# Kernel tuning notes

Hardware: AMD Instinct MI355X
Metric: run time of the kernel (lower is better)

## Reference

```python
import jax, jax.numpy as jnp
import numpy as np

N, E, B, L = 32768, 524288, 64, 512  # nodes, edges, graphs, max nodes/graph
V, D, H = 10000, 256, 512            # vocab, embed_dim, hidden_dim


def gcn_conv(h, W, b, src, dst, n):
    """PyG GCNConv: add self-loops, symmetric deg normalization, scatter-sum."""
    h = h @ W  # [n, out]
    loops = jnp.arange(n)
    s = jnp.concatenate([src, loops])
    d = jnp.concatenate([dst, loops])
    deg = jax.ops.segment_sum(jnp.ones_like(d, dtype=h.dtype), d, num_segments=n)
    dinv = jnp.where(deg > 0, jax.lax.rsqrt(deg), 0.0)
    norm = dinv[s] * dinv[d]  # [E+n]
    out = jax.ops.segment_sum(h[s] * norm[:, None], d, num_segments=n)
    return out + b


def gru_seq(x, Wih, Whh, bih, bhh):
    """torch nn.GRU (1 layer, batch_first). x: [B, T, H] -> outputs [T, B, H]."""
    def step(h, x_t):
        gi = x_t @ Wih.T + bih          # [B, 3H]
        gh = h @ Whh.T + bhh            # [B, 3H]
        ir, iz, inn = jnp.split(gi, 3, axis=-1)
        hr, hz, hn = jnp.split(gh, 3, axis=-1)
        r = jax.nn.sigmoid(ir + hr)
        z = jax.nn.sigmoid(iz + hz)
        n = jnp.tanh(inn + r * hn)
        h = (1.0 - z) * n + z * h
        return h, h
    h0 = jnp.zeros((x.shape[0], Whh.shape[1]), x.dtype)
    _, outs = jax.lax.scan(step, h0, jnp.swapaxes(x, 0, 1))
    return outs  # [T, B, H]


def setup_inputs() -> dict:
    key = jax.random.key(0)
    ks = jax.random.split(key, 16)
    s = 0.05
    x = jax.random.randint(ks[0], (N,), 0, V)
    edge_index = jax.random.randint(ks[1], (2, E), 0, N)
    batch_idx = jnp.arange(N) // L  # sorted graph ids, L nodes per graph
    focal_points = jax.random.uniform(ks[2], (B, 1), jnp.float32)
    return {
        "x": x, "edge_index": edge_index, "batch_idx": batch_idx,
        "focal_points": focal_points,
        "emb": jax.random.normal(ks[3], (V, D), jnp.float32) * s,
        "W1": jax.random.normal(ks[4], (D, H), jnp.float32) * s,
        "b1": jnp.zeros((H,), jnp.float32),
        "W2": jax.random.normal(ks[5], (H, H), jnp.float32) * s,
        "b2": jnp.zeros((H,), jnp.float32),
        "Wih": jax.random.normal(ks[6], (3 * H, H), jnp.float32) * s,
        "Whh": jax.random.normal(ks[7], (3 * H, H), jnp.float32) * s,
        "bih": jnp.zeros((3 * H,), jnp.float32),
        "bhh": jnp.zeros((3 * H,), jnp.float32),
        "fc1_w": jax.random.normal(ks[8], (H + 1, H), jnp.float32) * s,
        "fc1_b": jnp.zeros((H,), jnp.float32),
        "fc2_w": jax.random.normal(ks[9], (H, 1), jnp.float32) * s,
        "fc2_b": jnp.zeros((1,), jnp.float32),
    }


def reference(x, edge_index, batch_idx, focal_points, emb, W1, b1, W2, b2,
              Wih, Whh, bih, bhh, fc1_w, fc1_b, fc2_w, fc2_b):
    src, dst = edge_index[0], edge_index[1]
    h = emb[x]  # [N, D]
    h = jax.nn.relu(gcn_conv(h, W1, b1, src, dst, N))
    h = jax.nn.relu(gcn_conv(h, W2, b2, src, dst, N))  # [N, H]

    # Ragged -> padded: scatter each node to (graph, position-within-graph)
    ones = jnp.ones((N,), h.dtype)
    counts = jax.ops.segment_sum(ones, batch_idx, num_segments=B)
    starts = jnp.cumsum(counts) - counts  # exclusive cumsum
    pos = jnp.arange(N) - starts[batch_idx].astype(jnp.int32)
    padded = jnp.zeros((B, L, H), h.dtype).at[batch_idx, pos].set(h)

    gru_out = gru_seq(padded, Wih, Whh, bih, bhh)   # [L, B, H]
    graph_emb = gru_out.mean(axis=0)                # [B, H]
    g = jnp.concatenate([graph_emb, focal_points], axis=1)  # [B, H+1]
    out = jax.nn.relu(g @ fc1_w + fc1_b)
    out = jax.nn.sigmoid(out @ fc2_w + fc2_b)       # [B, 1]
    return out
```

## Files before the change

### kernel.cpp

```cpp
#include <hip/hip_runtime.h>

#define NODES 32768
#define EDGES 524288
#define BGR   64
#define LSEQ  512
#define DEMB  256
#define HDIM  512

typedef unsigned short u16;
typedef unsigned int   u32;
typedef unsigned long long u64;
typedef __attribute__((ext_vector_type(8))) short short8;
typedef __attribute__((ext_vector_type(4))) float f32x4;

__device__ __forceinline__ float bf2f(u16 u){ u32 x = ((u32)u)<<16; float f; __builtin_memcpy(&f,&x,4); return f; }
__device__ __forceinline__ u16 f2bf(float f){ u32 x; __builtin_memcpy(&x,&f,4); u32 r = x + 0x7fffu + ((x>>16)&1u); return (u16)(r>>16); }
__device__ __forceinline__ float lo16(u32 u){ u32 x = u<<16; float f; __builtin_memcpy(&f,&x,4); return f; }
__device__ __forceinline__ float hi16(u32 u){ u32 x = u & 0xffff0000u; float f; __builtin_memcpy(&f,&x,4); return f; }
__device__ __forceinline__ u32 pack2(float a, float b){ return (u32)f2bf(a) | ((u32)f2bf(b)<<16); }


__global__ void zero_i32(int* p, int n){
  int i = blockIdx.x*256 + threadIdx.x;
  if (i < n) p[i] = 0;
}

__global__ void transpose_cast(const float* __restrict__ in, u16* __restrict__ out, int K, int N){
  int i = blockIdx.x*256 + threadIdx.x;
  if (i < N*K){ int n = i / K, k = i - n*K; out[i] = f2bf(in[(size_t)k*N + n]); }
}

__global__ void cast_bf(const float* __restrict__ in, u16* __restrict__ out, int n){
  int i = blockIdx.x*256 + threadIdx.x;
  if (i < n) out[i] = f2bf(in[i]);
}

__global__ void count_indeg(const int* __restrict__ dst, int* __restrict__ indeg){
  int e = blockIdx.x*256 + threadIdx.x;
  if (e < EDGES) atomicAdd(&indeg[dst[e]], 1);
}

__global__ void compute_dinv(const int* __restrict__ indeg, float* __restrict__ dinv){
  int i = blockIdx.x*256 + threadIdx.x;
  if (i < NODES) dinv[i] = rsqrtf((float)(indeg[i] + 1));
}

__global__ __launch_bounds__(1024) void scan_csr(const int* __restrict__ indeg,
                                                 int* __restrict__ row_ptr,
                                                 int* __restrict__ cursor){
  __shared__ int part[1024];
  int tid = threadIdx.x, base = tid*32;
  int loc[32]; int s = 0;
  for (int i=0;i<32;i++){ loc[i] = s; s += indeg[base+i]; }
  part[tid] = s; __syncthreads();
  for (int off=1; off<1024; off<<=1){
    int v = part[tid]; int add = (tid>=off) ? part[tid-off] : 0;
    __syncthreads(); part[tid] = v + add; __syncthreads();
  }
  int offt = (tid==0) ? 0 : part[tid-1];
  for (int i=0;i<32;i++){ int v = offt + loc[i]; row_ptr[base+i] = v; cursor[base+i] = v; }
}

__global__ void fill_csr(const int* __restrict__ src, const int* __restrict__ dst,
                         int* __restrict__ cursor, int* __restrict__ csr_src){
  int e = blockIdx.x*256 + threadIdx.x;
  if (e < EDGES){ int d = dst[e]; int p = atomicAdd(&cursor[d], 1); csr_src[p] = src[e]; }
}

__global__ __launch_bounds__(256) void agg_emb(const int* __restrict__ x, const u16* __restrict__ embb,
    const float* __restrict__ dinv, const int* __restrict__ row_ptr, const int* __restrict__ indeg,
    const int* __restrict__ csr_src, u16* __restrict__ out){
  int node = blockIdx.x*4 + (threadIdx.x>>6);
  int lane = threadIdx.x & 63;
  float di = dinv[node];
  int xi = x[node];
  u64 hv = *(const u64*)(embb + (size_t)xi*DEMB + lane*4);
  u32 h0 = (u32)hv, h1 = (u32)(hv>>32);
  float a0 = lo16(h0)*di, a1 = hi16(h0)*di, a2 = lo16(h1)*di, a3 = hi16(h1)*di;
  int st = row_ptr[node], cn = indeg[node];
  for (int p = st; p < st+cn; p++){
    int s = csr_src[p];
    float ws = dinv[s];
    u64 v = *(const u64*)(embb + (size_t)x[s]*DEMB + lane*4);
    u32 w0 = (u32)v, w1 = (u32)(v>>32);
    a0 += lo16(w0)*ws; a1 += hi16(w0)*ws; a2 += lo16(w1)*ws; a3 += hi16(w1)*ws;
  }
  u64 pv = (u64)pack2(a0*di,a1*di) | ((u64)pack2(a2*di,a3*di)<<32);
  *(u64*)(out + (size_t)node*DEMB + lane*4) = pv;
}

__global__ __launch_bounds__(256) void agg_h(const u16* __restrict__ hin, const float* __restrict__ dinv,
    const int* __restrict__ row_ptr, const int* __restrict__ indeg,
    const int* __restrict__ csr_src, u16* __restrict__ out){
  int node = blockIdx.x*4 + (threadIdx.x>>6);
  int lane = threadIdx.x & 63;
  float di = dinv[node];
  float a[8];
  uint4 hv = *((const uint4*)(hin + (size_t)node*HDIM) + lane);
  a[0]=lo16(hv.x)*di; a[1]=hi16(hv.x)*di; a[2]=lo16(hv.y)*di; a[3]=hi16(hv.y)*di;
  a[4]=lo16(hv.z)*di; a[5]=hi16(hv.z)*di; a[6]=lo16(hv.w)*di; a[7]=hi16(hv.w)*di;
  int st = row_ptr[node], cn = indeg[node];
  for (int p = st; p < st+cn; p++){
    int s = csr_src[p];
    float ws = dinv[s];
    uint4 v = *((const uint4*)(hin + (size_t)s*HDIM) + lane);
    a[0]+=lo16(v.x)*ws; a[1]+=hi16(v.x)*ws; a[2]+=lo16(v.y)*ws; a[3]+=hi16(v.y)*ws;
    a[4]+=lo16(v.z)*ws; a[5]+=hi16(v.z)*ws; a[6]+=lo16(v.w)*ws; a[7]+=hi16(v.w)*ws;
  }
  uint4 o; o.x=pack2(a[0]*di,a[1]*di); o.y=pack2(a[2]*di,a[3]*di);
  o.z=pack2(a[4]*di,a[5]*di); o.w=pack2(a[6]*di,a[7]*di);
  *(uint4*)(out + (size_t)node*HDIM + lane*8) = o;
}

#define BM 128
#define BN 128
#define BKK 32
__global__ __launch_bounds__(256) void gemm_bt(const u16* __restrict__ A, const u16* __restrict__ BT,
    const float* __restrict__ bias, u16* __restrict__ C, int M, int N, int K, int relu){
  __shared__ u16 aS[BM][BKK+8];
  __shared__ u16 bS[BN][BKK+8];
  int tid = threadIdx.x;
  int m0 = blockIdx.y * BM, n0 = blockIdx.x * BN;
  int lane = tid & 63, w = tid >> 6;
  int wm = w >> 1, wn = w & 1;
  f32x4 acc[4][4];
  for (int i=0;i<4;i++) for (int j=0;j<4;j++) acc[i][j] = (f32x4)0.0f;

  int r  = tid >> 1;
  int cc = (tid & 1) * 16;
  const u16* Ag = A + (size_t)(m0 + r) * K + cc;
  const u16* Bg = BT + (size_t)(n0 + r) * K + cc;
  int l15 = lane & 15, q8 = (lane >> 4) * 8;

  for (int k0 = 0; k0 < K; k0 += BKK) {
    uint4 av0 = *(const uint4*)(Ag + k0);
    uint4 av1 = *(const uint4*)(Ag + k0 + 8);
    uint4 bv0 = *(const uint4*)(Bg + k0);
    uint4 bv1 = *(const uint4*)(Bg + k0 + 8);
    *(uint4*)&aS[r][cc]   = av0; *(uint4*)&aS[r][cc+8] = av1;
    *(uint4*)&bS[r][cc]   = bv0; *(uint4*)&bS[r][cc+8] = bv1;
    __syncthreads();
    short8 af[4], bfr[4];
    for (int i=0;i<4;i++) af[i]  = *(const short8*)&aS[wm*64 + i*16 + l15][q8];
    for (int j=0;j<4;j++) bfr[j] = *(const short8*)&bS[wn*64 + j*16 + l15][q8];
    for (int i=0;i<4;i++)
      for (int j=0;j<4;j++)
        acc[i][j] = __builtin_amdgcn_mfma_f32_16x16x32_bf16(af[i], bfr[j], acc[i][j], 0, 0, 0);
    __syncthreads();
  }
  int q = lane >> 4;
  for (int i=0;i<4;i++) for (int j=0;j<4;j++){
    int col = n0 + wn*64 + j*16 + l15;
    float bval = bias[col];
    for (int rr=0; rr<4; rr++){
      int row = m0 + wm*64 + i*16 + q*4 + rr;
      float v = acc[i][j][rr] + bval;
      if (relu) v = fmaxf(v, 0.f);
      C[(size_t)row * N + col] = f2bf(v);
    }
  }
}

__global__ __launch_bounds__(512) void gru_kernel(const u16* __restrict__ gi,
    const float* __restrict__ Whh, const float* __restrict__ bhh,
    float* __restrict__ graph_emb, u64* __restrict__ xbuf){
  __shared__ u16  w_lds[96*520];
  __shared__ u16  h_lds[16*520];
  __shared__ float gh_lds[16*100];

  int tid = threadIdx.x;
  int g = blockIdx.x >> 4, j = blockIdx.x & 15;
  int lane = tid & 63, wave = tid >> 6;

  for (int idx = tid; idx < 96*512; idx += 512){
    int rr = idx >> 9, c = idx & 511;
    int grow = (rr >> 5) * 512 + j*32 + (rr & 31);
    w_lds[rr*520 + c] = f2bf(Whh[(size_t)grow*512 + c]);
  }
  for (int idx = tid; idx < 16*520; idx += 512) h_lds[idx] = 0;

  int b = tid >> 5, hh = tid & 31;
  int bg = g*16 + b;
  int c_r = j*32 + hh, c_z = 512 + j*32 + hh, c_n = 1024 + j*32 + hh;
  float bias_r = bhh[c_r], bias_z = bhh[c_z], bias_n = bhh[c_n];
  const u16* gi_row = gi + (size_t)bg * LSEQ * 1536;
  float h_prev = 0.f, accm = 0.f;
  int l15 = lane & 15, q8 = (lane>>4)*8, qr = (lane>>4)*4;

  u64* xb = xbuf + (size_t)g * 8192;
  u16 g_r = gi_row[c_r], g_z = gi_row[c_z], g_n = gi_row[c_n];

  __syncthreads();

  for (int t = 0; t < LSEQ; t++){
    if (wave < 6){
      f32x4 acc0 = (f32x4)0.0f, acc1 = (f32x4)0.0f;
      const u16* wrow = &w_lds[(wave*16 + l15)*520];
      const u16* hrow = &h_lds[l15*520];
      #pragma unroll
      for (int k0 = 0; k0 < 256; k0 += 32){
        acc0 = __builtin_amdgcn_mfma_f32_16x16x32_bf16(*(const short8*)(hrow + k0 + q8),
                                                       *(const short8*)(wrow + k0 + q8), acc0, 0, 0, 0);
        acc1 = __builtin_amdgcn_mfma_f32_16x16x32_bf16(*(const short8*)(hrow + 256 + k0 + q8),
                                                       *(const short8*)(wrow + 256 + k0 + q8), acc1, 0, 0, 0);
      }
      f32x4 acc = acc0 + acc1;
      int col = wave*16 + l15;
      #pragma unroll
      for (int rr2 = 0; rr2 < 4; rr2++) gh_lds[(qr + rr2)*100 + col] = acc[rr2];
    }
    __syncthreads();

    float ghr = gh_lds[b*100 + hh]      + bias_r;
    float ghz = gh_lds[b*100 + 32 + hh] + bias_z;
    float ghn = gh_lds[b*100 + 64 + hh] + bias_n;
    float rg = 1.f / (1.f + __expf(-(bf2f(g_r) + ghr)));
    float zg = 1.f / (1.f + __expf(-(bf2f(g_z) + ghz)));
    float pre = bf2f(g_n) + rg * ghn;
    pre = fminf(fmaxf(pre, -20.f), 20.f);
    float e2 = __expf(2.f * pre);
    float nn = (e2 - 1.f) / (e2 + 1.f);
    float h_new = (1.f - zg) * nn + zg * h_prev;
    accm += h_new; h_prev = h_new;

    u32 tag = (u32)(t + 1);
    float h_nb = __shfl_xor(h_new, 1, 64);
    if ((hh & 1) == 0){
      u64 val = ((u64)tag << 32) | (u64)pack2(h_new, h_nb);
      __hip_atomic_store(xb + (size_t)((t&1)*16 + b)*256 + j*16 + (hh>>1), val,
                         __ATOMIC_RELAXED, __HIP_MEMORY_SCOPE_AGENT);
    }

    int tn = (t + 1 < LSEQ) ? t + 1 : t;
    const u16* gp2 = gi_row + (size_t)tn * 1536;
    u16 n_r = gp2[c_r], n_z = gp2[c_z], n_n = gp2[c_n];

    const u64* rp = xb + (size_t)((t&1)*16 + b)*256 + hh*8;
    u64 v[8];
    bool ok;
    do {
      #pragma unroll
      for (int i=0;i<8;i++) v[i] = __hip_atomic_load(rp + i, __ATOMIC_RELAXED, __HIP_MEMORY_SCOPE_AGENT);
      ok = true;
      #pragma unroll
      for (int i=0;i<8;i++) ok = ok && ((u32)(v[i] >> 32) == tag);
    } while (!ok);

    u32* hl = (u32*)h_lds + b*260 + hh*8;
    #pragma unroll
    for (int i=0;i<8;i++) hl[i] = (u32)v[i];
    __syncthreads();

    g_r = n_r; g_z = n_z; g_n = n_n;
  }
  graph_emb[(size_t)bg*512 + j*32 + hh] = accm * (1.f/512.f);
}

__global__ __launch_bounds__(256) void head(const float* __restrict__ graph_emb, const float* __restrict__ focal,
    const float* __restrict__ fc1w, const float* __restrict__ fc1b,
    const float* __restrict__ fc2w, const float* __restrict__ fc2b, float* __restrict__ out){
  __shared__ float gv[513];
  __shared__ float h1s[512];
  __shared__ float red[4];
  int bq = blockIdx.x, tid = threadIdx.x;
  for (int i = tid; i < 512; i += 256) gv[i] = graph_emb[(size_t)bq*512 + i];
  if (tid == 0) gv[512] = focal[bq];
  __syncthreads();
  for (int c = tid; c < 512; c += 256){
    float acc = fc1b[c];
    for (int k = 0; k < 513; k++) acc += gv[k] * fc1w[(size_t)k*512 + c];
    h1s[c] = fmaxf(acc, 0.f);
  }
  __syncthreads();
  float p = h1s[tid]*fc2w[tid] + h1s[tid+256]*fc2w[tid+256];
  for (int off = 32; off; off >>= 1) p += __shfl_down(p, off, 64);
  if ((tid & 63) == 0) red[tid >> 6] = p;
  __syncthreads();
  if (tid == 0){
    float s = red[0]+red[1]+red[2]+red[3] + fc2b[0];
    out[bq] = 1.f / (1.f + __expf(-s));
  }
}

extern "C" void kernel_launch(void* const* d_in, const int* in_sizes, int n_in,
                              void* d_out, int out_size, void* d_ws, size_t ws_size,
                              hipStream_t stream){
  const int*   x     = (const int*)d_in[0];
  const int*   edge  = (const int*)d_in[1];
  const int*   srcp  = edge;
  const int*   dstp  = edge + EDGES;
  const float* focal = (const float*)d_in[3];
  const float* emb   = (const float*)d_in[4];
  const float* W1    = (const float*)d_in[5];
  const float* b1    = (const float*)d_in[6];
  const float* W2    = (const float*)d_in[7];
  const float* b2    = (const float*)d_in[8];
  const float* Wih   = (const float*)d_in[9];
  const float* Whh   = (const float*)d_in[10];
  const float* bih   = (const float*)d_in[11];
  const float* bhh   = (const float*)d_in[12];
  const float* fc1w  = (const float*)d_in[13];
  const float* fc1b  = (const float*)d_in[14];
  const float* fc2w  = (const float*)d_in[15];
  const float* fc2b  = (const float*)d_in[16];

  char* ws = (char*)d_ws;
  constexpr size_t H2_OFF    = 0;
  constexpr size_t AGG1_OFF  = 33554432;
  constexpr size_t H1_OFF    = 50331648;
  constexpr size_t AGG2_OFF  = 83886080;
  constexpr size_t GI_OFF    = 33554432;
  constexpr size_t MISC      = 134217728;
  constexpr size_t INDEG_OFF = MISC;
  constexpr size_t CNT_OFF   = MISC + 131072;
  constexpr size_t DINV_OFF  = MISC + 131328;
  constexpr size_t ROWPTR_OFF= MISC + 262400;
  constexpr size_t CURSOR_OFF= MISC + 393472;
  constexpr size_t CSR_OFF   = MISC + 524544;
  constexpr size_t W1T_OFF   = MISC + 2621696;
  constexpr size_t W2T_OFF   = MISC + 2883840;
  constexpr size_t WIHB_OFF  = MISC + 3408128;
  constexpr size_t XBUF_OFF  = MISC + 4980992;
  constexpr size_t GEMB_OFF  = MISC + 5243136;

  int*   indeg  = (int*)(ws + INDEG_OFF);
  float* dinv   = (float*)(ws + DINV_OFF);
  int*   rowptr = (int*)(ws + ROWPTR_OFF);
  int*   cursor = (int*)(ws + CURSOR_OFF);
  int*   csrsrc = (int*)(ws + CSR_OFF);
  u16*   W1T    = (u16*)(ws + W1T_OFF);
  u16*   W2T    = (u16*)(ws + W2T_OFF);
  u16*   WihB   = (u16*)(ws + WIHB_OFF);
  u16*   agg1   = (u16*)(ws + AGG1_OFF);
  u16*   h1     = (u16*)(ws + H1_OFF);
  u16*   agg2   = (u16*)(ws + AGG2_OFF);
  u16*   embb   = (u16*)(ws + AGG2_OFF);
  u16*   h2     = (u16*)(ws + H2_OFF);
  u16*   gi     = (u16*)(ws + GI_OFF);
  u64*   xbuf   = (u64*)(ws + XBUF_OFF);
  float* gemb   = (float*)(ws + GEMB_OFF);

  zero_i32<<<129, 256, 0, stream>>>(indeg, 32768 + 64);
  transpose_cast<<<512, 256, 0, stream>>>(W1, W1T, 256, 512);
  transpose_cast<<<1024, 256, 0, stream>>>(W2, W2T, 512, 512);
  cast_bf<<<3072, 256, 0, stream>>>(Wih, WihB, 1536*512);
  cast_bf<<<10000, 256, 0, stream>>>(emb, embb, 10000*256);
  count_indeg<<<2048, 256, 0, stream>>>(dstp, indeg);
  compute_dinv<<<128, 256, 0, stream>>>(indeg, dinv);
  scan_csr<<<1, 1024, 0, stream>>>(indeg, rowptr, cursor);
  fill_csr<<<2048, 256, 0, stream>>>(srcp, dstp, cursor, csrsrc);
  agg_emb<<<8192, 256, 0, stream>>>(x, embb, dinv, rowptr, indeg, csrsrc, agg1);
  gemm_bt<<<dim3(4, 256), 256, 0, stream>>>(agg1, W1T, b1, h1, NODES, 512, 256, 1);
  agg_h<<<8192, 256, 0, stream>>>(h1, dinv, rowptr, indeg, csrsrc, agg2);
  gemm_bt<<<dim3(4, 256), 256, 0, stream>>>(agg2, W2T, b2, h2, NODES, 512, 512, 1);
  gemm_bt<<<dim3(12, 256), 256, 0, stream>>>(h2, WihB, bih, gi, NODES, 1536, 512, 0);
  gru_kernel<<<64, 512, 0, stream>>>(gi, Whh, bhh, gemb, xbuf);
  head<<<64, 256, 0, stream>>>(gemb, focal, fc1w, fc1b, fc2w, fc2b, (float*)d_out);
}
```

Baseline: 2.587 ms.

## Interleave two batch groups per GRU block to hide inter-block exchange latency

```diff
diff --git a/kernel.cpp b/kernel.cpp
--- a/kernel.cpp
+++ b/kernel.cpp
@@ -165,95 +165,131 @@
     const float* __restrict__ Whh, const float* __restrict__ bhh,
     float* __restrict__ graph_emb, u64* __restrict__ xbuf){
   __shared__ u16  w_lds[96*520];
-  __shared__ u16  h_lds[16*520];
-  __shared__ float gh_lds[16*100];
+  __shared__ u16  hA_lds[16*520];
+  __shared__ u16  hB_lds[16*520];
+  __shared__ float ghA_lds[16*100];
+  __shared__ float ghB_lds[16*100];
 
   int tid = threadIdx.x;
-  int g = blockIdx.x >> 4, j = blockIdx.x & 15;
+  int tau = blockIdx.x >> 4, j = blockIdx.x & 15;
+  int gA = tau*2, gB = tau*2 + 1;
   int lane = tid & 63, wave = tid >> 6;
+  (void)lane;
 
   for (int idx = tid; idx < 96*512; idx += 512){
     int rr = idx >> 9, c = idx & 511;
     int grow = (rr >> 5) * 512 + j*32 + (rr & 31);
     w_lds[rr*520 + c] = f2bf(Whh[(size_t)grow*512 + c]);
   }
-  for (int idx = tid; idx < 16*520; idx += 512) h_lds[idx] = 0;
+  for (int idx = tid; idx < 16*520; idx += 512){ hA_lds[idx] = 0; hB_lds[idx] = 0; }
 
   int b = tid >> 5, hh = tid & 31;
-  int bg = g*16 + b;
+  int bgA = gA*16 + b, bgB = gB*16 + b;
   int c_r = j*32 + hh, c_z = 512 + j*32 + hh, c_n = 1024 + j*32 + hh;
   float bias_r = bhh[c_r], bias_z = bhh[c_z], bias_n = bhh[c_n];
-  const u16* gi_row = gi + (size_t)bg * LSEQ * 1536;
-  float h_prev = 0.f, accm = 0.f;
-  int l15 = lane & 15, q8 = (lane>>4)*8, qr = (lane>>4)*4;
-
-  u64* xb = xbuf + (size_t)g * 8192;
-  u16 g_r = gi_row[c_r], g_z = gi_row[c_z], g_n = gi_row[c_n];
+  const u16* giA = gi + (size_t)bgA * LSEQ * 1536;
+  const u16* giB = gi + (size_t)bgB * LSEQ * 1536;
+  float h_prevA = 0.f, accmA = 0.f;
+  float h_prevB = 0.f, accmB = 0.f;
+  int l15 = tid & 15, q8 = ((tid & 63)>>4)*8, qr = ((tid & 63)>>4)*4;
+
+  u64* xbA = xbuf + (size_t)gA * 8192;
+  u64* xbB = xbuf + (size_t)gB * 8192;
+  u16 gA_r = giA[c_r], gA_z = giA[c_z], gA_n = giA[c_n];
+  u16 gB_r = giB[c_r], gB_z = giB[c_z], gB_n = giB[c_n];
 
   __syncthreads();
 
+#define MATVEC(HLDS, GHLDS) do { \
+    f32x4 acc0 = (f32x4)0.0f, acc1 = (f32x4)0.0f; \
+    const u16* wrow = &w_lds[(wave*16 + l15)*520]; \
+    const u16* hrow = &HLDS[l15*520]; \
+    _Pragma("unroll") \
+    for (int k0 = 0; k0 < 256; k0 += 32){ \
+      acc0 = __builtin_amdgcn_mfma_f32_16x16x32_bf16(*(const short8*)(hrow + k0 + q8), \
+                                                     *(const short8*)(wrow + k0 + q8), acc0, 0, 0, 0); \
+      acc1 = __builtin_amdgcn_mfma_f32_16x16x32_bf16(*(const short8*)(hrow + 256 + k0 + q8), \
+                                                     *(const short8*)(wrow + 256 + k0 + q8), acc1, 0, 0, 0); \
+    } \
+    f32x4 acc = acc0 + acc1; \
+    int col = wave*16 + l15; \
+    _Pragma("unroll") \
+    for (int rr2 = 0; rr2 < 4; rr2++) GHLDS[(qr + rr2)*100 + col] = acc[rr2]; \
+  } while(0)
+
+#define GATES(GHLDS, GR, GZ, GN, HPREV, HNEW) do { \
+    float ghr = GHLDS[b*100 + hh]      + bias_r; \
+    float ghz = GHLDS[b*100 + 32 + hh] + bias_z; \
+    float ghn = GHLDS[b*100 + 64 + hh] + bias_n; \
+    float rg = 1.f / (1.f + __expf(-(bf2f(GR) + ghr))); \
+    float zg = 1.f / (1.f + __expf(-(bf2f(GZ) + ghz))); \
+    float pre = bf2f(GN) + rg * ghn; \
+    pre = fminf(fmaxf(pre, -20.f), 20.f); \
+    float e2 = __expf(2.f * pre); \
+    float nn = (e2 - 1.f) / (e2 + 1.f); \
+    HNEW = (1.f - zg) * nn + zg * HPREV; \
+  } while(0)
+
+#define PUBLISH(XB, HNEW) do { \
+    float h_nb = __shfl_xor(HNEW, 1, 64); \
+    if ((hh & 1) == 0){ \
+      u64 val = ((u64)tag << 32) | (u64)pack2(HNEW, h_nb); \
+      __hip_atomic_store(XB + (size_t)((t&1)*16 + b)*256 + j*16 + (hh>>1), val, \
+                         __ATOMIC_RELAXED, __HIP_MEMORY_SCOPE_AGENT); \
+    } \
+  } while(0)
+
+#define POLLCOMMIT(XB, HLDS) do { \
+    const u64* rp = XB + (size_t)((t&1)*16 + b)*256 + hh*8; \
+    u64 v[8]; bool ok; \
+    do { \
+      _Pragma("unroll") \
+      for (int i=0;i<8;i++) v[i] = __hip_atomic_load(rp + i, __ATOMIC_RELAXED, __HIP_MEMORY_SCOPE_AGENT); \
+      ok = true; \
+      _Pragma("unroll") \
+      for (int i=0;i<8;i++) ok = ok && ((u32)(v[i] >> 32) == tag); \
+    } while (!ok); \
+    u32* hl = (u32*)HLDS + b*260 + hh*8; \
+    _Pragma("unroll") \
+    for (int i=0;i<8;i++) hl[i] = (u32)v[i]; \
+  } while(0)
+
   for (int t = 0; t < LSEQ; t++){
-    if (wave < 6){
-      f32x4 acc0 = (f32x4)0.0f, acc1 = (f32x4)0.0f;
-      const u16* wrow = &w_lds[(wave*16 + l15)*520];
-      const u16* hrow = &h_lds[l15*520];
-      #pragma unroll
-      for (int k0 = 0; k0 < 256; k0 += 32){
-        acc0 = __builtin_amdgcn_mfma_f32_16x16x32_bf16(*(const short8*)(hrow + k0 + q8),
-                                                       *(const short8*)(wrow + k0 + q8), acc0, 0, 0, 0);
-        acc1 = __builtin_amdgcn_mfma_f32_16x16x32_bf16(*(const short8*)(hrow + 256 + k0 + q8),
-                                                       *(const short8*)(wrow + 256 + k0 + q8), acc1, 0, 0, 0);
-      }
-      f32x4 acc = acc0 + acc1;
-      int col = wave*16 + l15;
-      #pragma unroll
-      for (int rr2 = 0; rr2 < 4; rr2++) gh_lds[(qr + rr2)*100 + col] = acc[rr2];
-    }
-    __syncthreads();
-
-    float ghr = gh_lds[b*100 + hh]      + bias_r;
-    float ghz = gh_lds[b*100 + 32 + hh] + bias_z;
-    float ghn = gh_lds[b*100 + 64 + hh] + bias_n;
-    float rg = 1.f / (1.f + __expf(-(bf2f(g_r) + ghr)));
-    float zg = 1.f / (1.f + __expf(-(bf2f(g_z) + ghz)));
-    float pre = bf2f(g_n) + rg * ghn;
-    pre = fminf(fmaxf(pre, -20.f), 20.f);
-    float e2 = __expf(2.f * pre);
-    float nn = (e2 - 1.f) / (e2 + 1.f);
-    float h_new = (1.f - zg) * nn + zg * h_prev;
-    accm += h_new; h_prev = h_new;
-
     u32 tag = (u32)(t + 1);
-    float h_nb = __shfl_xor(h_new, 1, 64);
-    if ((hh & 1) == 0){
-      u64 val = ((u64)tag << 32) | (u64)pack2(h_new, h_nb);
-      __hip_atomic_store(xb + (size_t)((t&1)*16 + b)*256 + j*16 + (hh>>1), val,
-                         __ATOMIC_RELAXED, __HIP_MEMORY_SCOPE_AGENT);
-    }
-
     int tn = (t + 1 < LSEQ) ? t + 1 : t;
-    const u16* gp2 = gi_row + (size_t)tn * 1536;
-    u16 n_r = gp2[c_r], n_z = gp2[c_z], n_n = gp2[c_n];
-
-    const u64* rp = xb + (size_t)((t&1)*16 + b)*256 + hh*8;
-    u64 v[8];
-    bool ok;
-    do {
-      #pragma unroll
-      for (int i=0;i<8;i++) v[i] = __hip_atomic_load(rp + i, __ATOMIC_RELAXED, __HIP_MEMORY_SCOPE_AGENT);
-      ok = true;
-      #pragma unroll
-      for (int i=0;i<8;i++) ok = ok && ((u32)(v[i] >> 32) == tag);
-    } while (!ok);
-
-    u32* hl = (u32*)h_lds + b*260 + hh*8;
-    #pragma unroll
-    for (int i=0;i<8;i++) hl[i] = (u32)v[i];
-    __syncthreads();
-
-    g_r = n_r; g_z = n_z; g_n = n_n;
-  }
-  graph_emb[(size_t)bg*512 + j*32 + hh] = accm * (1.f/512.f);
+
+    if (wave < 6) MATVEC(hA_lds, ghA_lds);
+    __syncthreads();
+    float h_newA;
+    GATES(ghA_lds, gA_r, gA_z, gA_n, h_prevA, h_newA);
+    accmA += h_newA; h_prevA = h_newA;
+    PUBLISH(xbA, h_newA);
+    const u16* gpA = giA + (size_t)tn * 1536;
+    u16 nA_r = gpA[c_r], nA_z = gpA[c_z], nA_n = gpA[c_n];
+
+    if (wave < 6) MATVEC(hB_lds, ghB_lds);
+    __syncthreads();
+    float h_newB;
+    GATES(ghB_lds, gB_r, gB_z, gB_n, h_prevB, h_newB);
+    accmB += h_newB; h_prevB = h_newB;
+    PUBLISH(xbB, h_newB);
+    const u16* gpB = giB + (size_t)tn * 1536;
+    u16 nB_r = gpB[c_r], nB_z = gpB[c_z], nB_n = gpB[c_n];
+
+    POLLCOMMIT(xbA, hA_lds);
+    POLLCOMMIT(xbB, hB_lds);
+    __syncthreads();
+
+    gA_r = nA_r; gA_z = nA_z; gA_n = nA_n;
+    gB_r = nB_r; gB_z = nB_z; gB_n = nB_n;
+  }
+  graph_emb[(size_t)bgA*512 + j*32 + hh] = accmA * (1.f/512.f);
+  graph_emb[(size_t)bgB*512 + j*32 + hh] = accmB * (1.f/512.f);
+
+#undef MATVEC
+#undef GATES
+#undef PUBLISH
+#undef POLLCOMMIT
 }
 
 __global__ __launch_bounds__(256) void head(const float* __restrict__ graph_emb, const float* __restrict__ focal,
@@ -354,6 +390,6 @@
   agg_h<<<8192, 256, 0, stream>>>(h1, dinv, rowptr, indeg, csrsrc, agg2);
   gemm_bt<<<dim3(4, 256), 256, 0, stream>>>(agg2, W2T, b2, h2, NODES, 512, 512, 1);
   gemm_bt<<<dim3(12, 256), 256, 0, stream>>>(h2, WihB, bih, gi, NODES, 1536, 512, 0);
-  gru_kernel<<<64, 512, 0, stream>>>(gi, Whh, bhh, gemb, xbuf);
+  gru_kernel<<<32, 512, 0, stream>>>(gi, Whh, bhh, gemb, xbuf);
   head<<<64, 256, 0, stream>>>(gemb, focal, fc1w, fc1b, fc2w, fc2b, (float*)d_out);
 }
```

Result: slower. 3.569 ms (+38.0%).

## Replace per-element tagged exchange with flag-based cross-block barrier in GRU

Applied to the files above, without the earlier changes.

```diff
diff --git a/kernel.cpp b/kernel.cpp
--- a/kernel.cpp
+++ b/kernel.cpp
@@ -170,7 +170,7 @@
 
   int tid = threadIdx.x;
   int g = blockIdx.x >> 4, j = blockIdx.x & 15;
-  int lane = tid & 63, wave = tid >> 6;
+  int wave = tid >> 6;
 
   for (int idx = tid; idx < 96*512; idx += 512){
     int rr = idx >> 9, c = idx & 511;
@@ -185,14 +185,18 @@
   float bias_r = bhh[c_r], bias_z = bhh[c_z], bias_n = bhh[c_n];
   const u16* gi_row = gi + (size_t)bg * LSEQ * 1536;
   float h_prev = 0.f, accm = 0.f;
-  int l15 = lane & 15, q8 = (lane>>4)*8, qr = (lane>>4)*4;
-
-  u64* xb = xbuf + (size_t)g * 8192;
+  int l15 = tid & 15, q8 = ((tid & 63)>>4)*8, qr = ((tid & 63)>>4)*4;
+
+  u32* db = (u32*)xbuf;
+  u32* fb = (u32*)((char*)xbuf + 131072);
   u16 g_r = gi_row[c_r], g_z = gi_row[c_z], g_n = gi_row[c_n];
 
   __syncthreads();
 
   for (int t = 0; t < LSEQ; t++){
+    u32 tag = (u32)(t + 1);
+    int par = t & 1;
+
     if (wave < 6){
       f32x4 acc0 = (f32x4)0.0f, acc1 = (f32x4)0.0f;
       const u16* wrow = &w_lds[(wave*16 + l15)*520];
@@ -223,11 +227,10 @@
     float h_new = (1.f - zg) * nn + zg * h_prev;
     accm += h_new; h_prev = h_new;
 
-    u32 tag = (u32)(t + 1);
     float h_nb = __shfl_xor(h_new, 1, 64);
+    u32* dpar = db + (size_t)((g*2 + par)*16 + b)*256;
     if ((hh & 1) == 0){
-      u64 val = ((u64)tag << 32) | (u64)pack2(h_new, h_nb);
-      __hip_atomic_store(xb + (size_t)((t&1)*16 + b)*256 + j*16 + (hh>>1), val,
+      __hip_atomic_store(dpar + j*16 + (hh>>1), pack2(h_new, h_nb),
                          __ATOMIC_RELAXED, __HIP_MEMORY_SCOPE_AGENT);
     }
 
@@ -235,20 +238,30 @@
     const u16* gp2 = gi_row + (size_t)tn * 1536;
     u16 n_r = gp2[c_r], n_z = gp2[c_z], n_n = gp2[c_n];
 
-    const u64* rp = xb + (size_t)((t&1)*16 + b)*256 + hh*8;
-    u64 v[8];
-    bool ok;
-    do {
-      #pragma unroll
-      for (int i=0;i<8;i++) v[i] = __hip_atomic_load(rp + i, __ATOMIC_RELAXED, __HIP_MEMORY_SCOPE_AGENT);
-      ok = true;
-      #pragma unroll
-      for (int i=0;i<8;i++) ok = ok && ((u32)(v[i] >> 32) == tag);
-    } while (!ok);
-
+    __syncthreads();
+
+    if (tid == 0)
+      __hip_atomic_store(fb + ((g*2 + par)*16 + j)*16, tag,
+                         __ATOMIC_RELEASE, __HIP_MEMORY_SCOPE_AGENT);
+    if (tid < 16){
+      const u32* fp = fb + ((g*2 + par)*16 + tid)*16;
+      int spins = 0;
+      while (__hip_atomic_load(fp, __ATOMIC_RELAXED, __HIP_MEMORY_SCOPE_AGENT) != tag){
+        if (++spins > 65536) break;
+      }
+    }
+    __syncthreads();
+
+    const u64* rp = (const u64*)dpar + hh*4;
+    u64 v0 = __hip_atomic_load(rp + 0, __ATOMIC_RELAXED, __HIP_MEMORY_SCOPE_AGENT);
+    u64 v1 = __hip_atomic_load(rp + 1, __ATOMIC_RELAXED, __HIP_MEMORY_SCOPE_AGENT);
+    u64 v2 = __hip_atomic_load(rp + 2, __ATOMIC_RELAXED, __HIP_MEMORY_SCOPE_AGENT);
+    u64 v3 = __hip_atomic_load(rp + 3, __ATOMIC_RELAXED, __HIP_MEMORY_SCOPE_AGENT);
     u32* hl = (u32*)h_lds + b*260 + hh*8;
-    #pragma unroll
-    for (int i=0;i<8;i++) hl[i] = (u32)v[i];
+    hl[0] = (u32)v0; hl[1] = (u32)(v0>>32);
+    hl[2] = (u32)v1; hl[3] = (u32)(v1>>32);
+    hl[4] = (u32)v2; hl[5] = (u32)(v2>>32);
+    hl[6] = (u32)v3; hl[7] = (u32)(v3>>32);
     __syncthreads();
 
     g_r = n_r; g_z = n_z; g_n = n_n;
```

Result: no change. 2.620 ms (+1.3%).

## Co-locate GRU group blocks on one XCD and poll via L2-local flags

Applied to the files above, without the earlier changes.

```diff
diff --git a/kernel.cpp b/kernel.cpp
--- a/kernel.cpp
+++ b/kernel.cpp
@@ -18,6 +18,23 @@
 __device__ __forceinline__ float lo16(u32 u){ u32 x = u<<16; float f; __builtin_memcpy(&f,&x,4); return f; }
 __device__ __forceinline__ float hi16(u32 u){ u32 x = u & 0xffff0000u; float f; __builtin_memcpy(&f,&x,4); return f; }
 __device__ __forceinline__ u32 pack2(float a, float b){ return (u32)f2bf(a) | ((u32)f2bf(b)<<16); }
+
+__device__ __forceinline__ void poll8_sc0(const u64* p, u64* v){
+  asm volatile(
+    "global_load_dwordx2 %0, %8, off sc0\n\t"
+    "global_load_dwordx2 %1, %8, off offset:8 sc0\n\t"
+    "global_load_dwordx2 %2, %8, off offset:16 sc0\n\t"
+    "global_load_dwordx2 %3, %8, off offset:24 sc0\n\t"
+    "global_load_dwordx2 %4, %8, off offset:32 sc0\n\t"
+    "global_load_dwordx2 %5, %8, off offset:40 sc0\n\t"
+    "global_load_dwordx2 %6, %8, off offset:48 sc0\n\t"
+    "global_load_dwordx2 %7, %8, off offset:56 sc0\n\t"
+    "s_waitcnt vmcnt(0)"
+    : "=&v"(v[0]), "=&v"(v[1]), "=&v"(v[2]), "=&v"(v[3]),
+      "=&v"(v[4]), "=&v"(v[5]), "=&v"(v[6]), "=&v"(v[7])
+    : "v"(p)
+    : "memory");
+}
 
 
 __global__ void zero_i32(int* p, int n){
@@ -163,14 +180,15 @@
 
 __global__ __launch_bounds__(512) void gru_kernel(const u16* __restrict__ gi,
     const float* __restrict__ Whh, const float* __restrict__ bhh,
-    float* __restrict__ graph_emb, u64* __restrict__ xbuf){
+    float* __restrict__ graph_emb, u64* __restrict__ fdb_base, u64* __restrict__ adb_base){
   __shared__ u16  w_lds[96*520];
   __shared__ u16  h_lds[16*520];
   __shared__ float gh_lds[16*100];
 
+  int g = blockIdx.x & 7, j = blockIdx.x >> 3;
+  if (g >= 4) return;
   int tid = threadIdx.x;
-  int g = blockIdx.x >> 4, j = blockIdx.x & 15;
-  int lane = tid & 63, wave = tid >> 6;
+  int wave = tid >> 6;
 
   for (int idx = tid; idx < 96*512; idx += 512){
     int rr = idx >> 9, c = idx & 511;
@@ -185,14 +203,21 @@
   float bias_r = bhh[c_r], bias_z = bhh[c_z], bias_n = bhh[c_n];
   const u16* gi_row = gi + (size_t)bg * LSEQ * 1536;
   float h_prev = 0.f, accm = 0.f;
-  int l15 = lane & 15, q8 = (lane>>4)*8, qr = (lane>>4)*4;
-
-  u64* xb = xbuf + (size_t)g * 8192;
+  int l15 = tid & 15, q8 = ((tid & 63)>>4)*8, qr = ((tid & 63)>>4)*4;
+
+  u64* fdb = fdb_base + (size_t)g * 8192;
+  u64* adb = adb_base + (size_t)g * 8192;
   u16 g_r = gi_row[c_r], g_z = gi_row[c_z], g_n = gi_row[c_n];
 
+  bool usefast = true;
+  int  strikes = 0;
+
   __syncthreads();
 
   for (int t = 0; t < LSEQ; t++){
+    u32 tag = (u32)(t + 1);
+    int par = t & 1;
+
     if (wave < 6){
       f32x4 acc0 = (f32x4)0.0f, acc1 = (f32x4)0.0f;
       const u16* wrow = &w_lds[(wave*16 + l15)*520];
@@ -223,28 +248,45 @@
     float h_new = (1.f - zg) * nn + zg * h_prev;
     accm += h_new; h_prev = h_new;
 
-    u32 tag = (u32)(t + 1);
     float h_nb = __shfl_xor(h_new, 1, 64);
+    size_t slot = (size_t)(par*16 + b)*256 + j*16 + (hh>>1);
     if ((hh & 1) == 0){
       u64 val = ((u64)tag << 32) | (u64)pack2(h_new, h_nb);
-      __hip_atomic_store(xb + (size_t)((t&1)*16 + b)*256 + j*16 + (hh>>1), val,
-                         __ATOMIC_RELAXED, __HIP_MEMORY_SCOPE_AGENT);
+      __hip_atomic_store(fdb + slot, val, __ATOMIC_RELAXED, __HIP_MEMORY_SCOPE_WORKGROUP);
+      __hip_atomic_store(adb + slot, val, __ATOMIC_RELAXED, __HIP_MEMORY_SCOPE_AGENT);
     }
 
     int tn = (t + 1 < LSEQ) ? t + 1 : t;
     const u16* gp2 = gi_row + (size_t)tn * 1536;
     u16 n_r = gp2[c_r], n_z = gp2[c_z], n_n = gp2[c_n];
 
-    const u64* rp = xb + (size_t)((t&1)*16 + b)*256 + hh*8;
+    size_t rowoff = (size_t)(par*16 + b)*256 + hh*8;
+    const u64* rpf = fdb + rowoff;
+    const u64* rpa = adb + rowoff;
     u64 v[8];
-    bool ok;
-    do {
-      #pragma unroll
-      for (int i=0;i<8;i++) v[i] = __hip_atomic_load(rp + i, __ATOMIC_RELAXED, __HIP_MEMORY_SCOPE_AGENT);
-      ok = true;
-      #pragma unroll
-      for (int i=0;i<8;i++) ok = ok && ((u32)(v[i] >> 32) == tag);
-    } while (!ok);
+    bool got = false;
+    if (usefast){
+      int cap = (t == 0) ? 1024 : 64;
+      for (int it = 0; it < cap; it++){
+        poll8_sc0(rpf, v);
+        bool ok = true;
+        #pragma unroll
+        for (int i=0;i<8;i++) ok = ok && ((u32)(v[i] >> 32) == tag);
+        if (ok){ got = true; break; }
+      }
+      if (got) strikes = 0;
+      else if (++strikes >= 2) usefast = false;
+    }
+    if (!got){
+      int spins = 0; bool ok;
+      do {
+        #pragma unroll
+        for (int i=0;i<8;i++) v[i] = __hip_atomic_load(rpa + i, __ATOMIC_RELAXED, __HIP_MEMORY_SCOPE_AGENT);
+        ok = true;
+        #pragma unroll
+        for (int i=0;i<8;i++) ok = ok && ((u32)(v[i] >> 32) == tag);
+      } while (!ok && ++spins < 16384);
+    }
 
     u32* hl = (u32*)h_lds + b*260 + hh*8;
     #pragma unroll
@@ -321,7 +363,8 @@
   constexpr size_t W2T_OFF   = MISC + 2883840;
   constexpr size_t WIHB_OFF  = MISC + 3408128;
   constexpr size_t XBUF_OFF  = MISC + 4980992;
-  constexpr size_t GEMB_OFF  = MISC + 5243136;
+  constexpr size_t XBUF2_OFF = MISC + 5243136;
+  constexpr size_t GEMB_OFF  = MISC + 5505280;
 
   int*   indeg  = (int*)(ws + INDEG_OFF);
   float* dinv   = (float*)(ws + DINV_OFF);
@@ -337,7 +380,8 @@
   u16*   embb   = (u16*)(ws + AGG2_OFF);
   u16*   h2     = (u16*)(ws + H2_OFF);
   u16*   gi     = (u16*)(ws + GI_OFF);
-  u64*   xbuf   = (u64*)(ws + XBUF_OFF);
+  u64*   fdb    = (u64*)(ws + XBUF_OFF);
+  u64*   adb    = (u64*)(ws + XBUF2_OFF);
   float* gemb   = (float*)(ws + GEMB_OFF);
 
   zero_i32<<<129, 256, 0, stream>>>(indeg, 32768 + 64);
@@ -354,6 +398,6 @@
   agg_h<<<8192, 256, 0, stream>>>(h1, dinv, rowptr, indeg, csrsrc, agg2);
   gemm_bt<<<dim3(4, 256), 256, 0, stream>>>(agg2, W2T, b2, h2, NODES, 512, 512, 1);
   gemm_bt<<<dim3(12, 256), 256, 0, stream>>>(h2, WihB, bih, gi, NODES, 1536, 512, 0);
-  gru_kernel<<<64, 512, 0, stream>>>(gi, Whh, bhh, gemb, xbuf);
+  gru_kernel<<<128, 512, 0, stream>>>(gi, Whh, bhh, gemb, fdb, adb);
   head<<<64, 256, 0, stream>>>(gemb, focal, fc1w, fc1b, fc2w, fc2b, (float*)d_out);
 }
```

After: 9.552 ms. 269% more time.
